# Optimization experiments

Hardware: AMD Instinct MI355X
Metric: run time of the kernel (lower is better)

The kernel has to match this reference:

```python
import jax, jax.numpy as jnp
import numpy as np

N = 100000      # nodes
E = 1600000     # edges (avg degree 16)
F_IN = 256      # num_features
H2 = 128        # nhid * 2 (layer 1 width)
H = 64          # nhid (layer 2 width)
C = 10          # num_classes


def setup_inputs() -> dict:
    key = jax.random.key(0)
    ks = jax.random.split(key, 8)
    x = jax.random.normal(ks[0], (N, F_IN), dtype=jnp.float32)
    edge_index = jax.random.randint(ks[1], (2, E), 0, N, dtype=jnp.int64)
    W1 = jax.random.normal(ks[2], (F_IN, H2), dtype=jnp.float32) / np.float32(np.sqrt(F_IN))
    b1 = jnp.zeros((H2,), jnp.float32)
    W2 = jax.random.normal(ks[3], (H2, H), dtype=jnp.float32) / np.float32(np.sqrt(H2))
    b2 = jnp.zeros((H,), jnp.float32)
    Wl = jax.random.normal(ks[4], (H, C), dtype=jnp.float32) / np.float32(np.sqrt(H))
    bl = jnp.zeros((C,), jnp.float32)
    return {"x": x, "edge_index": edge_index, "W1": W1, "b1": b1,
            "W2": W2, "b2": b2, "Wl": Wl, "bl": bl}


def reference(x, edge_index, W1, b1, W2, b2, Wl, bl):
    # --- GCN normalization with self-loops (PyG GCNConv default) ---
    loops = jnp.arange(N, dtype=edge_index.dtype)
    src = jnp.concatenate([edge_index[0], loops])  # message sources
    dst = jnp.concatenate([edge_index[1], loops])  # message targets
    deg = jax.ops.segment_sum(jnp.ones(src.shape[0], x.dtype), dst, num_segments=N)
    dinv = jnp.where(deg > 0, jax.lax.rsqrt(deg), 0.0)
    norm = dinv[src] * dinv[dst]                   # [E+N]

    def gcn_conv(h, W, b):
        m = h @ W                                  # transform first (out_channels small)
        agg = jax.ops.segment_sum(m[src] * norm[:, None], dst, num_segments=N)
        return agg + b

    h = jax.nn.relu(gcn_conv(x, W1, b1))           # [N, H2]
    h = jax.nn.relu(gcn_conv(h, W2, b2))           # [N, H]
    logits = h @ Wl + bl                            # [N, C]
    return jax.nn.log_softmax(logits, axis=-1)
```

## Files before the change

kernel.cpp:

```cpp
#include <hip/hip_runtime.h>


typedef unsigned short ushort_t;
typedef unsigned int uint_t;
typedef __attribute__((ext_vector_type(8))) short short8;
typedef __attribute__((ext_vector_type(4))) float floatx4;

static __device__ __forceinline__ ushort_t f2bf(float f) {
    union { float f; uint_t u; } c; c.f = f;
    return (ushort_t)((c.u + 0x8000u) >> 16);
}
static __device__ __forceinline__ float bf2f(ushort_t h) {
    union { uint_t u; float f; } c; c.u = ((uint_t)h) << 16;
    return c.f;
}
static __device__ __forceinline__ float2 up2(uint_t p) {
    union { uint_t u; float f; } lo, hi;
    lo.u = p << 16; hi.u = p & 0xffff0000u;
    return make_float2(lo.f, hi.f);
}
static __device__ __forceinline__ uint_t pk2bf(float a, float b) {
    return ((uint_t)f2bf(b) << 16) | (uint_t)f2bf(a);
}
static __device__ __forceinline__ void ld_lds16(void* lds, const void* g) {
    __builtin_amdgcn_global_load_lds(
        (const __attribute__((address_space(1))) unsigned int*)g,
        (__attribute__((address_space(3))) unsigned int*)lds, 16, 0, 0);
}

#define NBMAX 800
#define ECAP  4096

__global__ __launch_bounds__(256) void hist_kernel(
    const int* __restrict__ dst, int* __restrict__ histG, int E, int NB) {
    __shared__ int h[NBMAX];
    for (int i = threadIdx.x; i < NB; i += 256) h[i] = 0;
    __syncthreads();
    int i8 = (blockIdx.x * 256 + threadIdx.x) * 8;
    if (i8 + 7 < E) {
        int4 d0 = *(const int4*)(dst + i8);
        int4 d1 = *(const int4*)(dst + i8 + 4);
        atomicAdd(&h[d0.x >> 7], 1);
        atomicAdd(&h[d0.y >> 7], 1);
        atomicAdd(&h[d0.z >> 7], 1);
        atomicAdd(&h[d0.w >> 7], 1);
        atomicAdd(&h[d1.x >> 7], 1);
        atomicAdd(&h[d1.y >> 7], 1);
        atomicAdd(&h[d1.z >> 7], 1);
        atomicAdd(&h[d1.w >> 7], 1);
    } else {
        for (int e = i8; e < E; e++) atomicAdd(&h[dst[e] >> 7], 1);
    }
    __syncthreads();
    int* out = histG + (size_t)blockIdx.x * NB;
    for (int i = threadIdx.x; i < NB; i += 256) out[i] = h[i];
}

__global__ __launch_bounds__(256) void scan_bucket(
    int* __restrict__ histG, int* __restrict__ totG, int GB, int NB) {
    __shared__ int s[256];
    const int b = blockIdx.x;
    const int t = threadIdx.x;
    int running = 0;
    int nch = (GB + 255) / 256;
    for (int c = 0; c < nch; c++) {
        int j = c * 256 + t;
        int v = (j < GB) ? histG[(size_t)j * NB + b] : 0;
        s[t] = v;
        __syncthreads();
        for (int off = 1; off < 256; off <<= 1) {
            int tmp = (t >= off) ? s[t - off] : 0;
            __syncthreads();
            s[t] += tmp;
            __syncthreads();
        }
        if (j < GB) histG[(size_t)j * NB + b] = s[t] - v + running;
        int ctot = s[255];
        __syncthreads();
        running += ctot;
    }
    if (t == 0) totG[b] = running;
}

__global__ void scan_tot(const int* __restrict__ totG, int* __restrict__ bbase,
                         int NB) {
    __shared__ int s[256];
    const int t = threadIdx.x;
    int running = 0;
    int nch = (NB + 255) / 256;
    for (int c = 0; c < nch; c++) {
        int j = c * 256 + t;
        int v = (j < NB) ? totG[j] : 0;
        s[t] = v;
        __syncthreads();
        for (int off = 1; off < 256; off <<= 1) {
            int tmp = (t >= off) ? s[t - off] : 0;
            __syncthreads();
            s[t] += tmp;
            __syncthreads();
        }
        if (j < NB) bbase[j] = s[t] - v + running;
        int ctot = s[255];
        __syncthreads();
        running += ctot;
    }
    if (t == 0) bbase[NB] = running;
}

__global__ __launch_bounds__(256) void scatter_kernel(
    const int* __restrict__ src, const int* __restrict__ dst,
    const int* __restrict__ histG, const int* __restrict__ bbase,
    int* __restrict__ packed, int E, int NB) {
    __shared__ int lbase[NBMAX];
    const int* row = histG + (size_t)blockIdx.x * NB;
    for (int i = threadIdx.x; i < NB; i += 256)
        lbase[i] = bbase[i] + row[i];
    __syncthreads();
    int i8 = (blockIdx.x * 256 + threadIdx.x) * 8;
    if (i8 + 7 < E) {
        int4 s0 = *(const int4*)(src + i8);
        int4 s1 = *(const int4*)(src + i8 + 4);
        int4 d0 = *(const int4*)(dst + i8);
        int4 d1 = *(const int4*)(dst + i8 + 4);
        int p;
        p = atomicAdd(&lbase[d0.x >> 7], 1); packed[p] = s0.x | ((d0.x & 127) << 17);
        p = atomicAdd(&lbase[d0.y >> 7], 1); packed[p] = s0.y | ((d0.y & 127) << 17);
        p = atomicAdd(&lbase[d0.z >> 7], 1); packed[p] = s0.z | ((d0.z & 127) << 17);
        p = atomicAdd(&lbase[d0.w >> 7], 1); packed[p] = s0.w | ((d0.w & 127) << 17);
        p = atomicAdd(&lbase[d1.x >> 7], 1); packed[p] = s1.x | ((d1.x & 127) << 17);
        p = atomicAdd(&lbase[d1.y >> 7], 1); packed[p] = s1.y | ((d1.y & 127) << 17);
        p = atomicAdd(&lbase[d1.z >> 7], 1); packed[p] = s1.z | ((d1.z & 127) << 17);
        p = atomicAdd(&lbase[d1.w >> 7], 1); packed[p] = s1.w | ((d1.w & 127) << 17);
    } else {
        for (int e = i8; e < E; e++) {
            int d = dst[e];
            int p = atomicAdd(&lbase[d >> 7], 1);
            packed[p] = src[e] | ((d & 127) << 17);
        }
    }
}

__global__ __launch_bounds__(256) void bucket_csr(
    const int* __restrict__ packed, const int* __restrict__ bbase,
    int* __restrict__ rowptr, int* __restrict__ csr,
    float* __restrict__ dinv, int N, int NB) {
    __shared__ int ebuf[ECAP];
    __shared__ int cnt[128];
    __shared__ int pl[128];
    __shared__ int s[256];
    const int b = blockIdx.x;
    const int t = threadIdx.x;
    const int lo = bbase[b];
    const int hi = bbase[b + 1];
    int m = hi - lo;
    if (m > ECAP) m = ECAP;
    for (int i = t; i < m; i += 256) ebuf[i] = packed[lo + i];
    if (t < 128) cnt[t] = 0;
    __syncthreads();
    for (int i = t; i < m; i += 256) atomicAdd(&cnt[ebuf[i] >> 17], 1);
    __syncthreads();
    const int node0 = b << 7;
    int c = (t < 128) ? cnt[t] : 0;
    if (t < 128 && node0 + t < N)
        dinv[node0 + t] = rsqrtf((float)(c + 1));
    s[t] = c;
    __syncthreads();
    for (int off = 1; off < 256; off <<= 1) {
        int tmp = (t >= off) ? s[t - off] : 0;
        __syncthreads();
        s[t] += tmp;
        __syncthreads();
    }
    int excl = s[t] - c;
    if (t < 128) {
        pl[t] = excl;
        if (node0 + t <= N) rowptr[node0 + t] = lo + excl;
    }
    __syncthreads();
    for (int i = t; i < m; i += 256) {
        int e = ebuf[i];
        int p = atomicAdd(&pl[e >> 17], 1);
        csr[lo + p] = e & 0x1FFFF;
    }
}

__global__ void wcvt2_kernel(const float* __restrict__ W1, const float* __restrict__ W2,
                             ushort_t* __restrict__ W1t, ushort_t* __restrict__ W2t) {
    int i = blockIdx.x * 256 + threadIdx.x;
    if (i < 256 * 128) {
        int k = i / 128, n = i % 128;
        W1t[n * 256 + k] = f2bf(W1[i]);
    }
    int j = i - 256 * 128;
    if (j >= 0 && j < 128 * 64) {
        int k = j / 64, n = j % 64;
        W2t[n * 128 + k] = f2bf(W2[j]);
    }
}

__global__ __launch_bounds__(256) void gemm1_mfma(
    const float* __restrict__ A, const ushort_t* __restrict__ Bt,
    const float* __restrict__ dinv, ushort_t* __restrict__ out, int M) {
    __shared__ ushort_t As[2][128 * 40];
    __shared__ ushort_t Bs[2][128 * 32];
    const int tid = threadIdx.x;
    const int l = tid & 63;
    const int wave = tid >> 6;
    const int wm = wave >> 1, wn = wave & 1;
    const int lrow = l & 15, hh = l >> 4;
    const int m0 = blockIdx.x * 128;

    const int srow = tid >> 1, sh = tid & 1;
    int grow = m0 + srow; if (grow >= M) grow = M - 1;
    const float* gA = A + (size_t)grow * 256 + sh * 16;
    const int wslot = srow * 40 + sh * 16;

    int aslot[4], bslot[4];
    #pragma unroll
    for (int mt = 0; mt < 4; mt++) {
        int r = wm * 64 + mt * 16 + lrow;
        aslot[mt] = r * 40 + hh * 8;
    }
    #pragma unroll
    for (int nt = 0; nt < 4; nt++) {
        int nc = wn * 64 + nt * 16 + lrow;
        bslot[nt] = (nc * 4 + (hh ^ ((nc >> 2) & 3))) * 8;
    }

    floatx4 acc[4][4];
    #pragma unroll
    for (int mt = 0; mt < 4; mt++)
        #pragma unroll
        for (int nt = 0; nt < 4; nt++)
            acc[mt][nt] = (floatx4){0.f, 0.f, 0.f, 0.f};

    float4 ar[4];
    auto loadA = [&](int k0) {
        #pragma unroll
        for (int i = 0; i < 4; i++)
            ar[i] = *(const float4*)(gA + k0 + i * 4);
    };
    auto writeA = [&](int buf) {
        uint4 q0, q1;
        q0.x = pk2bf(ar[0].x, ar[0].y); q0.y = pk2bf(ar[0].z, ar[0].w);
        q0.z = pk2bf(ar[1].x, ar[1].y); q0.w = pk2bf(ar[1].z, ar[1].w);
        q1.x = pk2bf(ar[2].x, ar[2].y); q1.y = pk2bf(ar[2].z, ar[2].w);
        q1.z = pk2bf(ar[3].x, ar[3].y); q1.w = pk2bf(ar[3].z, ar[3].w);
        *(uint4*)&As[buf][wslot] = q0;
        *(uint4*)&As[buf][wslot + 8] = q1;
    };
    auto stageB = [&](int buf, int k0) {
        #pragma unroll
        for (int i = 0; i < 2; i++) {
            int s = i * 256 + tid;
            int nn = s >> 2, cp = s & 3;
            int cg = cp ^ ((nn >> 2) & 3);
            ld_lds16(&Bs[buf][s * 8], Bt + (size_t)nn * 256 + k0 + cg * 8);
        }
    };

    loadA(0);
    stageB(0, 0);
    writeA(0);
    __syncthreads();

    int buf = 0;
    for (int kk = 0; kk < 8; kk++) {
        if (kk < 7) {
            loadA((kk + 1) * 32);
            stageB(buf ^ 1, (kk + 1) * 32);
        }
        short8 afr[4], bfr[4];
        #pragma unroll
        for (int mt = 0; mt < 4; mt++)
            afr[mt] = *(const short8*)&As[buf][aslot[mt]];
        #pragma unroll
        for (int nt = 0; nt < 4; nt++)
            bfr[nt] = *(const short8*)&Bs[buf][bslot[nt]];
        #pragma unroll
        for (int mt = 0; mt < 4; mt++)
            #pragma unroll
            for (int nt = 0; nt < 4; nt++)
                acc[mt][nt] = __builtin_amdgcn_mfma_f32_16x16x32_bf16(
                    afr[mt], bfr[nt], acc[mt][nt], 0, 0, 0);
        if (kk < 7) writeA(buf ^ 1);
        __syncthreads();
        buf ^= 1;
    }

    const int r0 = hh * 4;
    #pragma unroll
    for (int mt = 0; mt < 4; mt++) {
        int mbase = m0 + wm * 64 + mt * 16 + r0;
        float4 dv = *(const float4*)&dinv[mbase];
        float d[4] = {dv.x, dv.y, dv.z, dv.w};
        #pragma unroll
        for (int i = 0; i < 4; i++) {
            int m = mbase + i;
            if (m < M) {
                #pragma unroll
                for (int nt = 0; nt < 4; nt++)
                    out[(size_t)m * 128 + wn * 64 + nt * 16 + lrow] =
                        f2bf(acc[mt][nt][i] * d[i]);
            }
        }
    }
}

__global__ __launch_bounds__(256) void gemm2_mfma(
    const ushort_t* __restrict__ A, const ushort_t* __restrict__ Bt,
    const float* __restrict__ dinv, ushort_t* __restrict__ out, int M) {
    __shared__ ushort_t As[2][128 * 32];
    __shared__ ushort_t Bs[2][64 * 32];
    const int tid = threadIdx.x;
    const int l = tid & 63;
    const int wave = tid >> 6;
    const int wm = wave >> 1, wn = wave & 1;
    const int lrow = l & 15, hh = l >> 4;
    const int m0 = blockIdx.x * 128;

    int aslot[4], bslot[2];
    #pragma unroll
    for (int mt = 0; mt < 4; mt++) {
        int r = wm * 64 + mt * 16 + lrow;
        aslot[mt] = (r * 4 + (hh ^ ((r >> 2) & 3))) * 8;
    }
    #pragma unroll
    for (int nt = 0; nt < 2; nt++) {
        int nc = wn * 32 + nt * 16 + lrow;
        bslot[nt] = (nc * 4 + (hh ^ ((nc >> 2) & 3))) * 8;
    }

    floatx4 acc[4][2];
    #pragma unroll
    for (int mt = 0; mt < 4; mt++)
        #pragma unroll
        for (int nt = 0; nt < 2; nt++)
            acc[mt][nt] = (floatx4){0.f, 0.f, 0.f, 0.f};

    auto stage = [&](int buf, int k0) {
        #pragma unroll
        for (int i = 0; i < 2; i++) {
            int s = i * 256 + tid;
            int r = s >> 2, cp = s & 3;
            int cg = cp ^ ((r >> 2) & 3);
            int row = m0 + r; if (row >= M) row = M - 1;
            ld_lds16(&As[buf][s * 8], A + (size_t)row * 128 + k0 + cg * 8);
        }
        {
            int s = tid;
            int nn = s >> 2, cp = s & 3;
            int cg = cp ^ ((nn >> 2) & 3);
            ld_lds16(&Bs[buf][s * 8], Bt + (size_t)nn * 128 + k0 + cg * 8);
        }
    };

    stage(0, 0);
    __syncthreads();
    int buf = 0;
    for (int kk = 0; kk < 4; kk++) {
        if (kk < 3) stage(buf ^ 1, (kk + 1) * 32);
        short8 afr[4], bfr[2];
        #pragma unroll
        for (int mt = 0; mt < 4; mt++)
            afr[mt] = *(const short8*)&As[buf][aslot[mt]];
        #pragma unroll
        for (int nt = 0; nt < 2; nt++)
            bfr[nt] = *(const short8*)&Bs[buf][bslot[nt]];
        #pragma unroll
        for (int mt = 0; mt < 4; mt++)
            #pragma unroll
            for (int nt = 0; nt < 2; nt++)
                acc[mt][nt] = __builtin_amdgcn_mfma_f32_16x16x32_bf16(
                    afr[mt], bfr[nt], acc[mt][nt], 0, 0, 0);
        __syncthreads();
        buf ^= 1;
    }

    const int r0 = hh * 4;
    #pragma unroll
    for (int mt = 0; mt < 4; mt++) {
        int mbase = m0 + wm * 64 + mt * 16 + r0;
        float4 dv = *(const float4*)&dinv[mbase];
        float d[4] = {dv.x, dv.y, dv.z, dv.w};
        #pragma unroll
        for (int i = 0; i < 4; i++) {
            int m = mbase + i;
            if (m < M) {
                #pragma unroll
                for (int nt = 0; nt < 2; nt++)
                    out[(size_t)m * 64 + wn * 32 + nt * 16 + lrow] =
                        f2bf(acc[mt][nt][i] * d[i]);
            }
        }
    }
}

__global__ __launch_bounds__(256) void spmm_relu128(
    const ushort_t* __restrict__ Mm, const int* __restrict__ rowptr,
    const int* __restrict__ csr, const float* __restrict__ dinv,
    const float* __restrict__ bias, ushort_t* __restrict__ out, int n) {
    int v = (blockIdx.x * 256 + threadIdx.x) >> 6;
    int lane = threadIdx.x & 63;
    if (v >= n) return;
    int jb = rowptr[v], je = rowptr[v + 1];
    int cntn = je - jb;
    const char* Mb = (const char*)Mm;
    const uint_t loff = lane * 4;

    float2 accA = up2(*(const uint_t*)(Mb + ((size_t)v << 8) + loff));
    float2 accB = make_float2(0.f, 0.f);

    for (int base = 0; base < cntn; base += 64) {
        int m = cntn - base; if (m > 64) m = 64;
        int roff = (base + lane < cntn) ? (csr[jb + base + lane] << 8) : 0;
        int jj = 0;
        for (; jj + 16 <= m; jj += 16) {
            uint_t o[16];
            #pragma unroll
            for (int t = 0; t < 16; t++) o[t] = (uint_t)__shfl(roff, jj + t) + loff;
            uint_t p[16];
            #pragma unroll
            for (int t = 0; t < 16; t++) p[t] = *(const uint_t*)(Mb + o[t]);
            #pragma unroll
            for (int t = 0; t < 16; t++) {
                float2 f = up2(p[t]);
                if (t & 1) { accB.x += f.x; accB.y += f.y; }
                else       { accA.x += f.x; accA.y += f.y; }
            }
        }
        for (; jj + 8 <= m; jj += 8) {
            uint_t o[8];
            #pragma unroll
            for (int t = 0; t < 8; t++) o[t] = (uint_t)__shfl(roff, jj + t) + loff;
            uint_t p[8];
            #pragma unroll
            for (int t = 0; t < 8; t++) p[t] = *(const uint_t*)(Mb + o[t]);
            #pragma unroll
            for (int t = 0; t < 8; t++) {
                float2 f = up2(p[t]);
                if (t & 1) { accB.x += f.x; accB.y += f.y; }
                else       { accA.x += f.x; accA.y += f.y; }
            }
        }
        for (; jj < m; jj++) {
            uint_t o = (uint_t)__shfl(roff, jj) + loff;
            float2 f = up2(*(const uint_t*)(Mb + o));
            accA.x += f.x; accA.y += f.y;
        }
    }
    float d = dinv[v];
    float2 bv = *(const float2*)&bias[lane * 2];
    float rx = fmaxf(d * (accA.x + accB.x) + bv.x, 0.f);
    float ry = fmaxf(d * (accA.y + accB.y) + bv.y, 0.f);
    uint_t packed = ((uint_t)f2bf(ry) << 16) | (uint_t)f2bf(rx);
    *(uint_t*)(out + (size_t)v * 128 + lane * 2) = packed;
}

__global__ __launch_bounds__(256) void spmm_relu64(
    const ushort_t* __restrict__ Mm, const int* __restrict__ rowptr,
    const int* __restrict__ csr, const float* __restrict__ dinv,
    const float* __restrict__ bias, ushort_t* __restrict__ out, int n) {
    int v = (blockIdx.x * 256 + threadIdx.x) >> 6;
    int lane = threadIdx.x & 63;
    if (v >= n) return;
    int jb = rowptr[v], je = rowptr[v + 1];
    int cntn = je - jb;
    const char* Mb = (const char*)Mm;
    const uint_t loff = lane * 2;

    float accA = bf2f(*(const ushort_t*)(Mb + ((size_t)v << 7) + loff));
    float accB = 0.f;

    for (int base = 0; base < cntn; base += 64) {
        int m = cntn - base; if (m > 64) m = 64;
        int roff = (base + lane < cntn) ? (csr[jb + base + lane] << 7) : 0;
        int jj = 0;
        for (; jj + 16 <= m; jj += 16) {
            uint_t o[16];
            #pragma unroll
            for (int t = 0; t < 16; t++) o[t] = (uint_t)__shfl(roff, jj + t) + loff;
            ushort_t p[16];
            #pragma unroll
            for (int t = 0; t < 16; t++) p[t] = *(const ushort_t*)(Mb + o[t]);
            #pragma unroll
            for (int t = 0; t < 16; t++) {
                if (t & 1) accB += bf2f(p[t]);
                else       accA += bf2f(p[t]);
            }
        }
        for (; jj + 8 <= m; jj += 8) {
            uint_t o[8];
            #pragma unroll
            for (int t = 0; t < 8; t++) o[t] = (uint_t)__shfl(roff, jj + t) + loff;
            ushort_t p[8];
            #pragma unroll
            for (int t = 0; t < 8; t++) p[t] = *(const ushort_t*)(Mb + o[t]);
            #pragma unroll
            for (int t = 0; t < 8; t++) {
                if (t & 1) accB += bf2f(p[t]);
                else       accA += bf2f(p[t]);
            }
        }
        for (; jj < m; jj++) {
            uint_t o = (uint_t)__shfl(roff, jj) + loff;
            accA += bf2f(*(const ushort_t*)(Mb + o));
        }
    }
    float r = fmaxf(dinv[v] * (accA + accB) + bias[lane], 0.f);
    out[(size_t)v * 64 + lane] = f2bf(r);
}

__global__ __launch_bounds__(256) void head_kernel(
    const ushort_t* __restrict__ h2, const float* __restrict__ Wl,
    const float* __restrict__ bl, float* __restrict__ out, int n) {
    __shared__ float Ws[64 * 10];
    __shared__ float bs[10];
    for (int i = threadIdx.x; i < 640; i += 256) Ws[i] = Wl[i];
    if (threadIdx.x < 10) bs[threadIdx.x] = bl[threadIdx.x];
    __syncthreads();
    int v = blockIdx.x * 256 + threadIdx.x;
    if (v >= n) return;
    float acc[10];
    #pragma unroll
    for (int c = 0; c < 10; c++) acc[c] = bs[c];
    const ushort_t* hrow = &h2[(size_t)v * 64];
    #pragma unroll
    for (int k0 = 0; k0 < 64; k0 += 8) {
        short8 hv = *(const short8*)&hrow[k0];
        #pragma unroll
        for (int kk = 0; kk < 8; kk++) {
            float hf = bf2f((ushort_t)hv[kk]);
            #pragma unroll
            for (int c = 0; c < 10; c++)
                acc[c] += hf * Ws[(k0 + kk) * 10 + c];
        }
    }
    float m = acc[0];
    #pragma unroll
    for (int c = 1; c < 10; c++) m = fmaxf(m, acc[c]);
    float s = 0.f;
    #pragma unroll
    for (int c = 0; c < 10; c++) s += expf(acc[c] - m);
    float lse = logf(s);
    #pragma unroll
    for (int c = 0; c < 10; c++) out[(size_t)v * 10 + c] = acc[c] - m - lse;
}

extern "C" void kernel_launch(void* const* d_in, const int* in_sizes, int n_in,
                              void* d_out, int out_size, void* d_ws, size_t ws_size,
                              hipStream_t stream) {
    const float* x   = (const float*)d_in[0];
    const int*   ei  = (const int*)d_in[1];
    const float* W1  = (const float*)d_in[2];
    const float* b1  = (const float*)d_in[3];
    const float* W2  = (const float*)d_in[4];
    const float* b2  = (const float*)d_in[5];
    const float* Wl  = (const float*)d_in[6];
    const float* bl  = (const float*)d_in[7];
    float*       out = (float*)d_out;

    const int N = in_sizes[0] / 256;
    const int E = in_sizes[1] / 2;
    const int* srcI = ei;
    const int* dstI = ei + E;

    const int NB = (N + 127) >> 7;
    const int GB = (E + 2047) / 2048;

    char* ws = (char*)d_ws;
    size_t off = 0;
    auto alloc = [&](size_t bytes) -> void* {
        void* p = ws + off;
        off = (off + bytes + 255) & ~(size_t)255;
        return p;
    };
    int*      histG  = (int*)alloc((size_t)GB * NB * 4);
    int*      totG   = (int*)alloc((size_t)NB * 4);
    int*      bbase  = (int*)alloc((size_t)(NB + 1) * 4);
    int*      packed = (int*)alloc((size_t)E * 4);
    int*      rowptr = (int*)alloc((size_t)(N + 1) * 4);
    float*    dinv   = (float*)alloc((size_t)(N + 128) * 4);
    int*      csr    = (int*)alloc((size_t)E * 4);
    ushort_t* W1t    = (ushort_t*)alloc((size_t)128 * 256 * 2);
    ushort_t* W2t    = (ushort_t*)alloc((size_t)64 * 128 * 2);
    ushort_t* bufA   = (ushort_t*)alloc((size_t)N * 128 * 2);
    ushort_t* bufB   = (ushort_t*)alloc((size_t)N * 128 * 2);

    hist_kernel<<<GB, 256, 0, stream>>>(dstI, histG, E, NB);
    scan_bucket<<<NB, 256, 0, stream>>>(histG, totG, GB, NB);
    scan_tot<<<1, 256, 0, stream>>>(totG, bbase, NB);
    scatter_kernel<<<GB, 256, 0, stream>>>(srcI, dstI, histG, bbase, packed, E, NB);
    bucket_csr<<<NB, 256, 0, stream>>>(packed, bbase, rowptr, csr, dinv, N, NB);

    wcvt2_kernel<<<(256 * 128 + 128 * 64 + 255) / 256, 256, 0, stream>>>(W1, W2, W1t, W2t);

    const int gblk = (N + 127) / 128;
    gemm1_mfma<<<gblk, 256, 0, stream>>>(x, W1t, dinv, bufA, N);
    spmm_relu128<<<(N + 3) / 4, 256, 0, stream>>>(bufA, rowptr, csr, dinv, b1, bufB, N);
    gemm2_mfma<<<gblk, 256, 0, stream>>>(bufB, W2t, dinv, bufA, N);
    spmm_relu64<<<(N + 3) / 4, 256, 0, stream>>>(bufA, rowptr, csr, dinv, b2, bufB, N);
    head_kernel<<<(N + 255) / 256, 256, 0, stream>>>(bufB, Wl, bl, out, N);
}
```

Baseline: 371.9 us.

## Gather neighbor rows with 16-byte loads across lane slots in SpMM kernels

Both SpMM kernels are restructured so that each lane loads 16 bytes (8 bf16 values) of a neighbor row. A wave now processes 4 neighbors at a time (128-wide) or 8 neighbors (64-wide) in parallel slots, and the partial sums are combined with xor shuffles at the end. Tail neighbors are padded to point at a zeroed dummy row, which removes the scalar remainder loops, and hipMemsetAsync clears that row. The aim is fewer, wider memory instructions and more neighbor-level parallelism per wave. The cost is a cross-lane reduction, extra memset launches, and only a quarter or eighth of the lanes doing the final write.

```diff
diff --git a/kernel.cpp b/kernel.cpp
--- a/kernel.cpp
+++ b/kernel.cpp
@@ -399,116 +399,155 @@
 __global__ __launch_bounds__(256) void spmm_relu128(
     const ushort_t* __restrict__ Mm, const int* __restrict__ rowptr,
     const int* __restrict__ csr, const float* __restrict__ dinv,
-    const float* __restrict__ bias, ushort_t* __restrict__ out, int n) {
+    const float* __restrict__ bias, ushort_t* __restrict__ out, int n, int doff) {
     int v = (blockIdx.x * 256 + threadIdx.x) >> 6;
     int lane = threadIdx.x & 63;
     if (v >= n) return;
-    int jb = rowptr[v], je = rowptr[v + 1];
-    int cntn = je - jb;
+    int jb = rowptr[v];
+    int cntn = rowptr[v + 1] - jb;
     const char* Mb = (const char*)Mm;
-    const uint_t loff = lane * 4;
-
-    float2 accA = up2(*(const uint_t*)(Mb + ((size_t)v << 8) + loff));
-    float2 accB = make_float2(0.f, 0.f);
+    const int slot = lane >> 4;
+    const int q = lane & 15;
+    const uint_t qb = (uint_t)q * 16;
+
+    float2 a0 = {0.f, 0.f}, a1 = a0, a2 = a0, a3 = a0;
+    if (slot == 0) {
+        uint4 s = *(const uint4*)(Mb + ((size_t)v << 8) + qb);
+        a0 = up2(s.x); a1 = up2(s.y); a2 = up2(s.z); a3 = up2(s.w);
+    }
 
     for (int base = 0; base < cntn; base += 64) {
         int m = cntn - base; if (m > 64) m = 64;
-        int roff = (base + lane < cntn) ? (csr[jb + base + lane] << 8) : 0;
+        int roff = (base + lane < cntn) ? (csr[jb + base + lane] << 8) : doff;
+        int m4 = (m + 3) & ~3;
         int jj = 0;
-        for (; jj + 16 <= m; jj += 16) {
-            uint_t o[16];
-            #pragma unroll
-            for (int t = 0; t < 16; t++) o[t] = (uint_t)__shfl(roff, jj + t) + loff;
-            uint_t p[16];
-            #pragma unroll
-            for (int t = 0; t < 16; t++) p[t] = *(const uint_t*)(Mb + o[t]);
-            #pragma unroll
-            for (int t = 0; t < 16; t++) {
-                float2 f = up2(p[t]);
-                if (t & 1) { accB.x += f.x; accB.y += f.y; }
-                else       { accA.x += f.x; accA.y += f.y; }
+        for (; jj + 16 <= m4; jj += 16) {
+            uint_t o[4];
+            #pragma unroll
+            for (int t = 0; t < 4; t++)
+                o[t] = (uint_t)__shfl(roff, jj + 4 * t + slot) + qb;
+            uint4 p[4];
+            #pragma unroll
+            for (int t = 0; t < 4; t++) p[t] = *(const uint4*)(Mb + o[t]);
+            #pragma unroll
+            for (int t = 0; t < 4; t++) {
+                float2 f;
+                f = up2(p[t].x); a0.x += f.x; a0.y += f.y;
+                f = up2(p[t].y); a1.x += f.x; a1.y += f.y;
+                f = up2(p[t].z); a2.x += f.x; a2.y += f.y;
+                f = up2(p[t].w); a3.x += f.x; a3.y += f.y;
             }
         }
-        for (; jj + 8 <= m; jj += 8) {
-            uint_t o[8];
-            #pragma unroll
-            for (int t = 0; t < 8; t++) o[t] = (uint_t)__shfl(roff, jj + t) + loff;
-            uint_t p[8];
-            #pragma unroll
-            for (int t = 0; t < 8; t++) p[t] = *(const uint_t*)(Mb + o[t]);
-            #pragma unroll
-            for (int t = 0; t < 8; t++) {
-                float2 f = up2(p[t]);
-                if (t & 1) { accB.x += f.x; accB.y += f.y; }
-                else       { accA.x += f.x; accA.y += f.y; }
-            }
-        }
-        for (; jj < m; jj++) {
-            uint_t o = (uint_t)__shfl(roff, jj) + loff;
-            float2 f = up2(*(const uint_t*)(Mb + o));
-            accA.x += f.x; accA.y += f.y;
-        }
-    }
-    float d = dinv[v];
-    float2 bv = *(const float2*)&bias[lane * 2];
-    float rx = fmaxf(d * (accA.x + accB.x) + bv.x, 0.f);
-    float ry = fmaxf(d * (accA.y + accB.y) + bv.y, 0.f);
-    uint_t packed = ((uint_t)f2bf(ry) << 16) | (uint_t)f2bf(rx);
-    *(uint_t*)(out + (size_t)v * 128 + lane * 2) = packed;
+        for (; jj < m4; jj += 4) {
+            uint_t o = (uint_t)__shfl(roff, jj + slot) + qb;
+            uint4 p = *(const uint4*)(Mb + o);
+            float2 f;
+            f = up2(p.x); a0.x += f.x; a0.y += f.y;
+            f = up2(p.y); a1.x += f.x; a1.y += f.y;
+            f = up2(p.z); a2.x += f.x; a2.y += f.y;
+            f = up2(p.w); a3.x += f.x; a3.y += f.y;
+        }
+    }
+    float r[8] = {a0.x, a0.y, a1.x, a1.y, a2.x, a2.y, a3.x, a3.y};
+    #pragma unroll
+    for (int i = 0; i < 8; i++) r[i] += __shfl_xor(r[i], 16);
+    #pragma unroll
+    for (int i = 0; i < 8; i++) r[i] += __shfl_xor(r[i], 32);
+    if (slot == 0) {
+        float d = dinv[v];
+        float4 bv0 = *(const float4*)&bias[q * 8];
+        float4 bv1 = *(const float4*)&bias[q * 8 + 4];
+        float o0 = fmaxf(d * r[0] + bv0.x, 0.f);
+        float o1 = fmaxf(d * r[1] + bv0.y, 0.f);
+        float o2 = fmaxf(d * r[2] + bv0.z, 0.f);
+        float o3 = fmaxf(d * r[3] + bv0.w, 0.f);
+        float o4 = fmaxf(d * r[4] + bv1.x, 0.f);
+        float o5 = fmaxf(d * r[5] + bv1.y, 0.f);
+        float o6 = fmaxf(d * r[6] + bv1.z, 0.f);
+        float o7 = fmaxf(d * r[7] + bv1.w, 0.f);
+        uint4 pk;
+        pk.x = pk2bf(o0, o1); pk.y = pk2bf(o2, o3);
+        pk.z = pk2bf(o4, o5); pk.w = pk2bf(o6, o7);
+        *(uint4*)(out + (size_t)v * 128 + q * 8) = pk;
+    }
 }
 
 __global__ __launch_bounds__(256) void spmm_relu64(
     const ushort_t* __restrict__ Mm, const int* __restrict__ rowptr,
     const int* __restrict__ csr, const float* __restrict__ dinv,
-    const float* __restrict__ bias, ushort_t* __restrict__ out, int n) {
+    const float* __restrict__ bias, ushort_t* __restrict__ out, int n, int doff) {
     int v = (blockIdx.x * 256 + threadIdx.x) >> 6;
     int lane = threadIdx.x & 63;
     if (v >= n) return;
-    int jb = rowptr[v], je = rowptr[v + 1];
-    int cntn = je - jb;
+    int jb = rowptr[v];
+    int cntn = rowptr[v + 1] - jb;
     const char* Mb = (const char*)Mm;
-    const uint_t loff = lane * 2;
-
-    float accA = bf2f(*(const ushort_t*)(Mb + ((size_t)v << 7) + loff));
-    float accB = 0.f;
+    const int slot = lane >> 3;
+    const int q = lane & 7;
+    const uint_t qb = (uint_t)q * 16;
+
+    float2 a0 = {0.f, 0.f}, a1 = a0, a2 = a0, a3 = a0;
+    if (slot == 0) {
+        uint4 s = *(const uint4*)(Mb + ((size_t)v << 7) + qb);
+        a0 = up2(s.x); a1 = up2(s.y); a2 = up2(s.z); a3 = up2(s.w);
+    }
 
     for (int base = 0; base < cntn; base += 64) {
         int m = cntn - base; if (m > 64) m = 64;
-        int roff = (base + lane < cntn) ? (csr[jb + base + lane] << 7) : 0;
+        int roff = (base + lane < cntn) ? (csr[jb + base + lane] << 7) : doff;
+        int m8 = (m + 7) & ~7;
         int jj = 0;
-        for (; jj + 16 <= m; jj += 16) {
-            uint_t o[16];
-            #pragma unroll
-            for (int t = 0; t < 16; t++) o[t] = (uint_t)__shfl(roff, jj + t) + loff;
-            ushort_t p[16];
-            #pragma unroll
-            for (int t = 0; t < 16; t++) p[t] = *(const ushort_t*)(Mb + o[t]);
-            #pragma unroll
-            for (int t = 0; t < 16; t++) {
-                if (t & 1) accB += bf2f(p[t]);
-                else       accA += bf2f(p[t]);
+        for (; jj + 16 <= m8; jj += 16) {
+            uint_t o[2];
+            #pragma unroll
+            for (int t = 0; t < 2; t++)
+                o[t] = (uint_t)__shfl(roff, jj + 8 * t + slot) + qb;
+            uint4 p[2];
+            #pragma unroll
+            for (int t = 0; t < 2; t++) p[t] = *(const uint4*)(Mb + o[t]);
+            #pragma unroll
+            for (int t = 0; t < 2; t++) {
+                float2 f;
+                f = up2(p[t].x); a0.x += f.x; a0.y += f.y;
+                f = up2(p[t].y); a1.x += f.x; a1.y += f.y;
+                f = up2(p[t].z); a2.x += f.x; a2.y += f.y;
+                f = up2(p[t].w); a3.x += f.x; a3.y += f.y;
             }
         }
-        for (; jj + 8 <= m; jj += 8) {
-            uint_t o[8];
-            #pragma unroll
-            for (int t = 0; t < 8; t++) o[t] = (uint_t)__shfl(roff, jj + t) + loff;
-            ushort_t p[8];
-            #pragma unroll
-            for (int t = 0; t < 8; t++) p[t] = *(const ushort_t*)(Mb + o[t]);
-            #pragma unroll
-            for (int t = 0; t < 8; t++) {
-                if (t & 1) accB += bf2f(p[t]);
-                else       accA += bf2f(p[t]);
-            }
-        }
-        for (; jj < m; jj++) {
-            uint_t o = (uint_t)__shfl(roff, jj) + loff;
-            accA += bf2f(*(const ushort_t*)(Mb + o));
-        }
-    }
-    float r = fmaxf(dinv[v] * (accA + accB) + bias[lane], 0.f);
-    out[(size_t)v * 64 + lane] = f2bf(r);
+        for (; jj < m8; jj += 8) {
+            uint_t o = (uint_t)__shfl(roff, jj + slot) + qb;
+            uint4 p = *(const uint4*)(Mb + o);
+            float2 f;
+            f = up2(p.x); a0.x += f.x; a0.y += f.y;
+            f = up2(p.y); a1.x += f.x; a1.y += f.y;
+            f = up2(p.z); a2.x += f.x; a2.y += f.y;
+            f = up2(p.w); a3.x += f.x; a3.y += f.y;
+        }
+    }
+    float r[8] = {a0.x, a0.y, a1.x, a1.y, a2.x, a2.y, a3.x, a3.y};
+    #pragma unroll
+    for (int i = 0; i < 8; i++) r[i] += __shfl_xor(r[i], 8);
+    #pragma unroll
+    for (int i = 0; i < 8; i++) r[i] += __shfl_xor(r[i], 16);
+    #pragma unroll
+    for (int i = 0; i < 8; i++) r[i] += __shfl_xor(r[i], 32);
+    if (slot == 0) {
+        float d = dinv[v];
+        float4 bv0 = *(const float4*)&bias[q * 8];
+        float4 bv1 = *(const float4*)&bias[q * 8 + 4];
+        float o0 = fmaxf(d * r[0] + bv0.x, 0.f);
+        float o1 = fmaxf(d * r[1] + bv0.y, 0.f);
+        float o2 = fmaxf(d * r[2] + bv0.z, 0.f);
+        float o3 = fmaxf(d * r[3] + bv0.w, 0.f);
+        float o4 = fmaxf(d * r[4] + bv1.x, 0.f);
+        float o5 = fmaxf(d * r[5] + bv1.y, 0.f);
+        float o6 = fmaxf(d * r[6] + bv1.z, 0.f);
+        float o7 = fmaxf(d * r[7] + bv1.w, 0.f);
+        uint4 pk;
+        pk.x = pk2bf(o0, o1); pk.y = pk2bf(o2, o3);
+        pk.z = pk2bf(o4, o5); pk.w = pk2bf(o6, o7);
+        *(uint4*)(out + (size_t)v * 64 + q * 8) = pk;
+    }
 }
 
 __global__ __launch_bounds__(256) void head_kernel(
@@ -584,7 +623,7 @@
     int*      csr    = (int*)alloc((size_t)E * 4);
     ushort_t* W1t    = (ushort_t*)alloc((size_t)128 * 256 * 2);
     ushort_t* W2t    = (ushort_t*)alloc((size_t)64 * 128 * 2);
-    ushort_t* bufA   = (ushort_t*)alloc((size_t)N * 128 * 2);
+    ushort_t* bufA   = (ushort_t*)alloc((size_t)(N + 2) * 128 * 2);
     ushort_t* bufB   = (ushort_t*)alloc((size_t)N * 128 * 2);
 
     hist_kernel<<<GB, 256, 0, stream>>>(dstI, histG, E, NB);
@@ -597,8 +636,10 @@
 
     const int gblk = (N + 127) / 128;
     gemm1_mfma<<<gblk, 256, 0, stream>>>(x, W1t, dinv, bufA, N);
-    spmm_relu128<<<(N + 3) / 4, 256, 0, stream>>>(bufA, rowptr, csr, dinv, b1, bufB, N);
+    hipMemsetAsync(bufA + (size_t)N * 128, 0, 256, stream);
+    spmm_relu128<<<(N + 3) / 4, 256, 0, stream>>>(bufA, rowptr, csr, dinv, b1, bufB, N, N << 8);
     gemm2_mfma<<<gblk, 256, 0, stream>>>(bufB, W2t, dinv, bufA, N);
-    spmm_relu64<<<(N + 3) / 4, 256, 0, stream>>>(bufA, rowptr, csr, dinv, b2, bufB, N);
+    hipMemsetAsync(bufA + (size_t)N * 64, 0, 128, stream);
+    spmm_relu64<<<(N + 3) / 4, 256, 0, stream>>>(bufA, rowptr, csr, dinv, b2, bufB, N, N << 7);
     head_kernel<<<(N + 255) / 256, 256, 0, stream>>>(bufB, Wl, bl, out, N);
 }
```

Result: faster. 362.7 us (-2.5%).
